# Kernel optimization log

Measured on AMD Instinct MI355X. Metric: run time of the kernel, lower is better.

The kernel has to match this reference:

```python
import jax, jax.numpy as jnp
import numpy as np

B, S, HID = 2, 2048, 2048
NH, NKV, HD = 8, 1, 256
G = NH // NKV  # key-value groups
ROPE_BASE = 10000.0


def _rope_tables(seq_len, dim, base=ROPE_BASE):
    inv_freq = 1.0 / (base ** (jnp.arange(0, dim, 2, dtype=jnp.float32) / dim))
    t = jnp.arange(seq_len, dtype=jnp.float32)
    freqs = jnp.outer(t, inv_freq)            # [S, dim/2]
    emb = jnp.concatenate([freqs, freqs], -1)  # [S, dim]
    return jnp.cos(emb), jnp.sin(emb)


def _rotate_half(x):
    x1, x2 = jnp.split(x, 2, axis=-1)
    return jnp.concatenate([-x2, x1], axis=-1)


def setup_inputs() -> dict:
    key = jax.random.key(0)
    ks = jax.random.split(key, 6)
    hidden_states = jax.random.normal(ks[0], (B, S, HID), dtype=jnp.float32)
    # additive causal mask (0 on/below diagonal, -1e9 above)
    causal = jnp.triu(jnp.full((S, S), -1e9, dtype=jnp.float32), k=1)
    attention_mask = jnp.broadcast_to(causal[None, None], (B, 1, S, S))
    sc = 0.02
    Wq = jax.random.normal(ks[1], (HID, NH * HD), dtype=jnp.float32) * sc
    Wk = jax.random.normal(ks[2], (HID, NKV * HD), dtype=jnp.float32) * sc
    Wv = jax.random.normal(ks[3], (HID, NKV * HD), dtype=jnp.float32) * sc
    Wo = jax.random.normal(ks[4], (NH * HD, HID), dtype=jnp.float32) * sc
    return {"hidden_states": hidden_states, "attention_mask": attention_mask,
            "Wq": Wq, "Wk": Wk, "Wv": Wv, "Wo": Wo}


def reference(hidden_states, attention_mask, Wq, Wk, Wv, Wo):
    b, s, _ = hidden_states.shape
    q = (hidden_states @ Wq).reshape(b, s, NH, HD).transpose(0, 2, 1, 3)    # [B,NH,S,D]
    k = (hidden_states @ Wk).reshape(b, s, NKV, HD).transpose(0, 2, 1, 3)   # [B,NKV,S,D]
    v = (hidden_states @ Wv).reshape(b, s, NKV, HD).transpose(0, 2, 1, 3)
    cos, sin = _rope_tables(s, HD)
    cos, sin = cos[None, None], sin[None, None]
    q = q * cos + _rotate_half(q) * sin
    k = k * cos + _rotate_half(k) * sin
    # GQA: broadcast KV over groups instead of repeat_interleave (same math)
    qg = q.reshape(b, NKV, G, s, HD)
    scores = jnp.einsum('bkgqd,bkld->bkgql', qg, k) / np.sqrt(HD)  # [B,NKV,G,S,S]
    scores = scores + attention_mask[:, :, None]                    # mask broadcast over kv/groups
    probs = jax.nn.softmax(scores, axis=-1)
    out = jnp.einsum('bkgql,bkld->bkgqd', probs, v)                 # [B,NKV,G,S,D]
    out = out.reshape(b, NH, s, HD).transpose(0, 2, 1, 3).reshape(b, s, NH * HD)
    return out @ Wo
```

## Files before the change

### kernel.cpp

```cpp
#include <hip/hip_runtime.h>
#include <hip/hip_bf16.h>
#include <cstdint>
#include <cstddef>

#define DEVI __device__ __forceinline__

typedef __attribute__((ext_vector_type(8))) short short8;
typedef __attribute__((ext_vector_type(4))) float f32x4;

constexpr int BB = 2, SS = 2048, HID = 2048, NH = 8, HD = 256;
constexpr int M_TOT = BB * SS;
constexpr int RTOT = BB * NH * SS;
constexpr float SM_SCALE_LOG2 = 0.09016844005556021f;

DEVI unsigned short f2bf(float f) {
  union { float f; unsigned int u; } v; v.f = f;
  unsigned int u = v.u;
  unsigned int r = (u + 0x7FFFu + ((u >> 16) & 1u)) >> 16;
  return (unsigned short)r;
}

DEVI float bf2f(unsigned short u) {
  union { unsigned int i; float f; } v; v.i = ((unsigned int)u) << 16;
  return v.f;
}

DEVI void gload_lds16(const void* g, void* l) {
  __builtin_amdgcn_global_load_lds(
      (const __attribute__((address_space(1))) unsigned int*)g,
      (__attribute__((address_space(3))) unsigned int*)l, 16, 0, 0);
}

__global__ void convert_f32_bf16(const float* __restrict__ in,
                                 unsigned short* __restrict__ out, int n8) {
  const int i = blockIdx.x * blockDim.x + threadIdx.x;
  if (i >= n8) return;
  const f32x4* p = (const f32x4*)in;
  f32x4 a = p[i * 2], b = p[i * 2 + 1];
  short8 o;
#pragma unroll
  for (int j = 0; j < 4; ++j) {
    o[j] = (short)f2bf(a[j]);
    o[j + 4] = (short)f2bf(b[j]);
  }
  ((short8*)out)[i] = o;
}

__global__ void transpose_w(const float* __restrict__ W,
                            unsigned short* __restrict__ Wt, int K, int N) {
  __shared__ float t[32][33];
  const int n0 = blockIdx.x * 32, k0 = blockIdx.y * 32;
  const int c = threadIdx.x & 31, r8 = threadIdx.x >> 5;
#pragma unroll
  for (int i = 0; i < 4; ++i) {
    const int r = r8 + i * 8;
    t[r][c] = W[(size_t)(k0 + r) * N + n0 + c];
  }
  __syncthreads();
#pragma unroll
  for (int i = 0; i < 4; ++i) {
    const int r = r8 + i * 8;
    Wt[(size_t)(n0 + r) * K + k0 + c] = f2bf(t[c][r]);
  }
}

__global__ void rope_table(float* __restrict__ ct, float* __restrict__ st) {
  const int i = blockIdx.x * blockDim.x + threadIdx.x;
  const int s = i >> 7, d = i & 127;
  const float inv = __expf(-(float)d * (9.210340371976184f / 128.0f));
  const float ang = (float)s * inv;
  float sn, cs;
  sincosf(ang, &sn, &cs);
  ct[i] = cs;
  st[i] = sn;
}

__global__ void rope_apply(unsigned short* __restrict__ X, const float* __restrict__ ct,
                           const float* __restrict__ st, int heads, int stride, int total) {
  const int i = blockIdx.x * blockDim.x + threadIdx.x;
  if (i >= total) return;
  const int d = i & 127;
  const int t = i >> 7;
  const int hh = t % heads;
  const int row = t / heads;
  const int s = row & (SS - 1);
  const size_t base = (size_t)row * stride + (size_t)hh * HD;
  const float q1 = bf2f(X[base + d]), q2 = bf2f(X[base + d + 128]);
  const float cs = ct[s * 128 + d], sn = st[s * 128 + d];
  X[base + d] = f2bf(q1 * cs - q2 * sn);
  X[base + d + 128] = f2bf(q2 * cs + q1 * sn);
}

template <int WMODE>
__global__ __launch_bounds__(256)
void gemm_bt(const unsigned short* __restrict__ A,
             const unsigned short* __restrict__ Bt,
             void* __restrict__ Cp, void* __restrict__ Cp2, void* __restrict__ Cp3,
             int N, int K) {
  __shared__ unsigned short As[128 * 64];
  __shared__ unsigned short Bs[128 * 64];
  const int tid = threadIdx.x;
  const int wid = tid >> 6, lane = tid & 63;
  const int wr = wid >> 1, wc = wid & 1;
  const int l15 = lane & 15, lg = lane >> 4;
  const int m0 = blockIdx.y * 128, n0 = blockIdx.x * 128;
  const int lrow = lane >> 3, lch = lane & 7;
  f32x4 acc[4][4];
#pragma unroll
  for (int i = 0; i < 4; ++i)
#pragma unroll
    for (int j = 0; j < 4; ++j) acc[i][j] = f32x4{0.f, 0.f, 0.f, 0.f};
  const unsigned short* Ab = A + (size_t)m0 * K;
  const unsigned short* Bb = Bt + (size_t)n0 * K;
  for (int k0 = 0; k0 < K; k0 += 64) {
    __syncthreads();
#pragma unroll
    for (int i = 0; i < 4; ++i) {
      const int r0 = wid * 32 + i * 8;
      const int r = r0 + lrow;
      gload_lds16(Ab + (size_t)r * K + k0 + ((lch ^ (r & 7)) * 8), &As[r0 * 64]);
      gload_lds16(Bb + (size_t)r * K + k0 + ((lch ^ (r & 7)) * 8), &Bs[r0 * 64]);
    }
    asm volatile("s_waitcnt vmcnt(0)" ::: "memory");
    __syncthreads();
#pragma unroll
    for (int kk = 0; kk < 2; ++kk) {
      short8 a[4], b[4];
#pragma unroll
      for (int m = 0; m < 4; ++m) {
        const int row = wr * 64 + m * 16 + l15;
        a[m] = *(const short8*)&As[row * 64 + (((kk * 4 + lg) ^ (row & 7)) * 8)];
      }
#pragma unroll
      for (int n = 0; n < 4; ++n) {
        const int row = wc * 64 + n * 16 + l15;
        b[n] = *(const short8*)&Bs[row * 64 + (((kk * 4 + lg) ^ (row & 7)) * 8)];
      }
#pragma unroll
      for (int m = 0; m < 4; ++m)
#pragma unroll
        for (int n = 0; n < 4; ++n)
          acc[m][n] = __builtin_amdgcn_mfma_f32_16x16x32_bf16(a[m], b[n], acc[m][n], 0, 0, 0);
    }
  }
  const int row0 = m0 + wr * 64 + lg * 4;
  const int col0 = n0 + wc * 64 + l15;
#pragma unroll
  for (int m = 0; m < 4; ++m)
#pragma unroll
    for (int n = 0; n < 4; ++n)
#pragma unroll
      for (int r = 0; r < 4; ++r) {
        const int row = row0 + m * 16 + r;
        const int col = col0 + n * 16;
        const float v = acc[m][n][r];
        if (WMODE == 1) {
          ((float*)Cp)[(size_t)row * N + col] = v;
        } else {
          if (col < 2048)
            ((unsigned short*)Cp)[(size_t)row * 2048 + col] = f2bf(v);
          else if (col < 2304)
            ((unsigned short*)Cp2)[(size_t)row * 256 + (col - 2048)] = f2bf(v);
          else
            ((unsigned short*)Cp3)[((size_t)((row >> 11) * HD + (col - 2304))) * SS + (row & (SS - 1))] = f2bf(v);
        }
      }
}

__global__ __launch_bounds__(512)
void attn_split(const unsigned short* __restrict__ Q,
                const unsigned short* __restrict__ Kc,
                const unsigned short* __restrict__ Vt,
                unsigned short* __restrict__ Opart, float* __restrict__ Ml) {
  __shared__ unsigned short Ks[2][64 * 256];
  __shared__ unsigned short Vs[2][256 * 64];
  __shared__ unsigned short Ps[8][1024];
  const int tid = threadIdx.x;
  const int wid = tid >> 6, lane = tid & 63;
  const int l15 = lane & 15, lg = lane >> 4;
  const int pi = (int)blockIdx.x >> 1, s = (int)blockIdx.x & 1;
  const int h = blockIdx.y, b = blockIdx.z;
  const int qtA = pi, qtB = 15 - pi;

  short8 qf[8];
  f32x4 acc[16];
  float mrow[4], lrow[4];

  auto load_q = [&](int qt) {
    const int qrow = qt * 128 + wid * 16 + l15;
    const size_t qbase = ((size_t)(b * SS + qrow)) * (NH * HD) + (size_t)h * HD;
#pragma unroll
    for (int c = 0; c < 8; ++c)
      qf[c] = *(const short8*)&Q[qbase + c * 32 + lg * 8];
#pragma unroll
    for (int n = 0; n < 16; ++n) acc[n] = f32x4{0.f, 0.f, 0.f, 0.f};
#pragma unroll
    for (int r = 0; r < 4; ++r) { mrow[r] = -3e38f; lrow[r] = 0.f; }
  };

  auto write_part = [&](int qt) {
    const size_t rbase = ((size_t)(b * NH + h)) * SS + qt * 128 + wid * 16 + lg * 4;
#pragma unroll
    for (int n = 0; n < 16; ++n)
#pragma unroll
      for (int r = 0; r < 4; ++r)
        Opart[((size_t)s * RTOT + rbase + r) * 256 + n * 16 + l15] = f2bf(acc[n][r]);
    if (l15 == 0) {
#pragma unroll
      for (int r = 0; r < 4; ++r)
        ((float2*)Ml)[(size_t)s * RTOT + rbase + r] = float2{mrow[r], lrow[r]};
    }
  };

  auto stage = [&](int buf, int kv0) {
    unsigned short* KsB = &Ks[buf][0];
    unsigned short* VsB = &Vs[buf][0];
#pragma unroll
    for (int j = 0; j < 4; ++j) {
      {
        const int r0 = wid * 8 + j * 2;
        const int r = r0 + (lane >> 5), c = lane & 31;
        gload_lds16(Kc + ((size_t)(b * SS + kv0 + r)) * HD + ((c ^ (r & 7)) * 8),
                    &KsB[r0 * 256]);
      }
      {
        const int r0 = (wid * 4 + j) * 8;
        const int r = r0 + (lane >> 3), c = lane & 7;
        gload_lds16(Vt + ((size_t)(b * HD + r)) * SS + kv0 + ((c ^ (r & 7)) * 8),
                    &VsB[r0 * 64]);
      }
    }
  };

  auto compute = [&](int buf, int qt, int kv0) {
    const int wmax = qt * 128 + wid * 16 + 15;
    if (kv0 > wmax) return;
    const unsigned short* KsB = &Ks[buf][0];
    const unsigned short* VsB = &Vs[buf][0];
    f32x4 sf[4];
    __builtin_amdgcn_s_setprio(1);
#pragma unroll
    for (int t = 0; t < 4; ++t) {
      f32x4 sv = {0.f, 0.f, 0.f, 0.f};
      const int kvr = t * 16 + l15;
      const char* krow = (const char*)KsB + kvr * 512;
      const int sw = (kvr & 7) << 4;
#pragma unroll
      for (int c = 0; c < 8; ++c) {
        short8 bf = *(const short8*)(krow + ((c * 64 + lg * 16) ^ sw));
        sv = __builtin_amdgcn_mfma_f32_16x16x32_bf16(qf[c], bf, sv, 0, 0, 0);
      }
      sf[t] = sv;
    }
    __builtin_amdgcn_s_setprio(0);

    float pm[4] = {-3e38f, -3e38f, -3e38f, -3e38f};
    const int qr0 = qt * 128 + wid * 16 + lg * 4;
#pragma unroll
    for (int t = 0; t < 4; ++t) {
      const int kvc = kv0 + t * 16 + l15;
#pragma unroll
      for (int r = 0; r < 4; ++r) {
        float v = sf[t][r] * SM_SCALE_LOG2;
        v = (kvc > qr0 + r) ? -3e38f : v;
        sf[t][r] = v;
        pm[r] = fmaxf(pm[r], v);
      }
    }
    float scale[4];
    float growth = -3e38f;
#pragma unroll
    for (int r = 0; r < 4; ++r) {
      float v = pm[r];
      v = fmaxf(v, __shfl_xor(v, 1));
      v = fmaxf(v, __shfl_xor(v, 2));
      v = fmaxf(v, __shfl_xor(v, 4));
      v = fmaxf(v, __shfl_xor(v, 8));
      pm[r] = v;
      growth = fmaxf(growth, v - mrow[r]);
    }
    const bool norescale = __all(growth <= 0.f);
#pragma unroll
    for (int r = 0; r < 4; ++r) {
      const float mn = norescale ? mrow[r] : fmaxf(mrow[r], pm[r]);
      scale[r] = norescale ? 1.f : exp2f(mrow[r] - mn);
      mrow[r] = mn;
      float sum = 0.f;
#pragma unroll
      for (int t = 0; t < 4; ++t) {
        const float p = exp2f(sf[t][r] - mn);
        sf[t][r] = p;
        sum += p;
      }
      sum += __shfl_xor(sum, 1);
      sum += __shfl_xor(sum, 2);
      sum += __shfl_xor(sum, 4);
      sum += __shfl_xor(sum, 8);
      lrow[r] = lrow[r] * scale[r] + sum;
    }
    if (!norescale) {
#pragma unroll
      for (int n = 0; n < 16; ++n)
#pragma unroll
        for (int r = 0; r < 4; ++r) acc[n][r] *= scale[r];
    }

    char* pw = (char*)&Ps[wid][0];
#pragma unroll
    for (int t = 0; t < 4; ++t)
#pragma unroll
      for (int r = 0; r < 4; ++r) {
        const int q = lg * 4 + r;
        *(unsigned short*)(pw + q * 128 + (((t * 16 + l15) * 2) ^ ((q & 7) << 4))) =
            f2bf(sf[t][r]);
      }
    asm volatile("s_waitcnt lgkmcnt(0)" ::: "memory");
    short8 pf[2];
    {
      const char* pr = pw + l15 * 128;
      const int sw = (l15 & 7) << 4;
      pf[0] = *(const short8*)(pr + ((lg * 16) ^ sw));
      pf[1] = *(const short8*)(pr + ((64 + lg * 16) ^ sw));
    }
    __builtin_amdgcn_s_setprio(1);
#pragma unroll
    for (int n = 0; n < 16; ++n) {
      const int dr = n * 16 + l15;
      const char* vrow = (const char*)VsB + dr * 128;
      const int sw = (dr & 7) << 4;
      short8 v0 = *(const short8*)(vrow + ((lg * 16) ^ sw));
      short8 v1 = *(const short8*)(vrow + ((64 + lg * 16) ^ sw));
      acc[n] = __builtin_amdgcn_mfma_f32_16x16x32_bf16(pf[0], v0, acc[n], 0, 0, 0);
      acc[n] = __builtin_amdgcn_mfma_f32_16x16x32_bf16(pf[1], v1, acc[n], 0, 0, 0);
    }
    __builtin_amdgcn_s_setprio(0);
  };

  auto kv_of = [&](int i) {
    const int j = (i <= qtA) ? i : (i - qtA - 1);
    return (s + 2 * j) * 64;
  };

  load_q(qtA);
  stage(0, kv_of(0));
  asm volatile("s_waitcnt vmcnt(0)" ::: "memory");
  __syncthreads();
  int buf = 0;
  for (int i = 0; i < 17; ++i) {
    if (i + 1 < 17) stage(buf ^ 1, kv_of(i + 1));
    if (i == qtA + 1) {
      write_part(qtA);
      load_q(qtB);
    }
    const int qt = (i <= qtA) ? qtA : qtB;
    compute(buf, qt, kv_of(i));
    asm volatile("s_waitcnt vmcnt(0)" ::: "memory");
    __syncthreads();
    buf ^= 1;
  }
  write_part(qtB);
}

__global__ void merge_splits(const unsigned short* __restrict__ Opart,
                             const float* __restrict__ Ml,
                             unsigned short* __restrict__ AO) {
  const int gid = blockIdx.x * 256 + threadIdx.x;
  const int ridx = gid >> 5;
  const int d0 = (gid & 31) * 8;
  const float2 ab0 = ((const float2*)Ml)[ridx];
  const float2 ab1 = ((const float2*)Ml)[RTOT + ridx];
  const float M = fmaxf(ab0.x, ab1.x);
  const float w0 = exp2f(ab0.x - M), w1 = exp2f(ab1.x - M);
  const float inv = 1.f / (w0 * ab0.y + w1 * ab1.y);
  const short8 p0 = *(const short8*)&Opart[(size_t)ridx * 256 + d0];
  const short8 p1 = *(const short8*)&Opart[((size_t)RTOT + ridx) * 256 + d0];
  const int b = ridx >> 14, rem = ridx & 16383;
  const int h = rem >> 11, srow = rem & 2047;
  short8 o;
#pragma unroll
  for (int j = 0; j < 8; ++j)
    o[j] = (short)f2bf((w0 * bf2f((unsigned short)p0[j]) +
                        w1 * bf2f((unsigned short)p1[j])) * inv);
  *(short8*)(AO + ((size_t)(b * SS + srow)) * (NH * HD) + (size_t)h * HD + d0) = o;
}

__global__ __launch_bounds__(256)
void attn_fb(const unsigned short* __restrict__ Q,
             const unsigned short* __restrict__ Kc,
             const unsigned short* __restrict__ Vt,
             unsigned short* __restrict__ AO) {
  __shared__ unsigned short Ks[2][64 * 256];
  __shared__ unsigned short Vs[2][256 * 64];
  __shared__ unsigned short Ps[4][1024];
  const int tid = threadIdx.x;
  const int wid = tid >> 6, lane = tid & 63;
  const int l15 = lane & 15, lg = lane >> 4;
  const int qtA = (int)blockIdx.x;
  const int qtB = 31 - qtA;
  const int h = blockIdx.y, b = blockIdx.z;

  short8 qf[8];
  f32x4 acc[16];
  float mrow[4], lrow[4];

  auto load_q = [&](int qt) {
    const int qrow = qt * 64 + wid * 16 + l15;
    const size_t qbase = ((size_t)(b * SS + qrow)) * (NH * HD) + (size_t)h * HD;
#pragma unroll
    for (int c = 0; c < 8; ++c)
      qf[c] = *(const short8*)&Q[qbase + c * 32 + lg * 8];
#pragma unroll
    for (int n = 0; n < 16; ++n) acc[n] = f32x4{0.f, 0.f, 0.f, 0.f};
#pragma unroll
    for (int r = 0; r < 4; ++r) { mrow[r] = -3e38f; lrow[r] = 0.f; }
  };

  auto write_o = [&](int qt) {
    float invl[4];
#pragma unroll
    for (int r = 0; r < 4; ++r) invl[r] = 1.f / lrow[r];
    const int orow0 = b * SS + qt * 64 + wid * 16 + lg * 4;
#pragma unroll
    for (int n = 0; n < 16; ++n)
#pragma unroll
      for (int r = 0; r < 4; ++r)
        AO[(size_t)(orow0 + r) * (NH * HD) + (size_t)h * HD + n * 16 + l15] =
            f2bf(acc[n][r] * invl[r]);
  };

  auto stage = [&](int buf, int kv0) {
    unsigned short* KsB = &Ks[buf][0];
    unsigned short* VsB = &Vs[buf][0];
#pragma unroll
    for (int j = 0; j < 8; ++j) {
      {
        const int r0 = wid * 16 + j * 2;
        const int r = r0 + (lane >> 5), c = lane & 31;
        gload_lds16(Kc + ((size_t)(b * SS + kv0 + r)) * HD + ((c ^ (r & 7)) * 8),
                    &KsB[r0 * 256]);
      }
      {
        const int r0 = (wid * 8 + j) * 8;
        const int r = r0 + (lane >> 3), c = lane & 7;
        gload_lds16(Vt + ((size_t)(b * HD + r)) * SS + kv0 + ((c ^ (r & 7)) * 8),
                    &VsB[r0 * 64]);
      }
    }
  };

  auto compute = [&](int buf, int qt, int kv0) {
    const int wmax = qt * 64 + wid * 16 + 15;
    if (kv0 > wmax) return;
    const unsigned short* KsB = &Ks[buf][0];
    const unsigned short* VsB = &Vs[buf][0];
    f32x4 sf[4];
#pragma unroll
    for (int t = 0; t < 4; ++t) {
      f32x4 sv = {0.f, 0.f, 0.f, 0.f};
      const int kvr = t * 16 + l15;
      const char* krow = (const char*)KsB + kvr * 512;
      const int sw = (kvr & 7) << 4;
#pragma unroll
      for (int c = 0; c < 8; ++c) {
        short8 bf = *(const short8*)(krow + ((c * 64 + lg * 16) ^ sw));
        sv = __builtin_amdgcn_mfma_f32_16x16x32_bf16(qf[c], bf, sv, 0, 0, 0);
      }
      sf[t] = sv;
    }
    float pm[4] = {-3e38f, -3e38f, -3e38f, -3e38f};
    const int qr0 = qt * 64 + wid * 16 + lg * 4;
#pragma unroll
    for (int t = 0; t < 4; ++t) {
      const int kvc = kv0 + t * 16 + l15;
#pragma unroll
      for (int r = 0; r < 4; ++r) {
        float v = sf[t][r] * 0.0625f;
        v = (kvc > qr0 + r) ? -3e38f : v;
        sf[t][r] = v;
        pm[r] = fmaxf(pm[r], v);
      }
    }
    float scale[4];
    float growth = -3e38f;
#pragma unroll
    for (int r = 0; r < 4; ++r) {
      float v = pm[r];
      v = fmaxf(v, __shfl_xor(v, 1));
      v = fmaxf(v, __shfl_xor(v, 2));
      v = fmaxf(v, __shfl_xor(v, 4));
      v = fmaxf(v, __shfl_xor(v, 8));
      pm[r] = v;
      growth = fmaxf(growth, v - mrow[r]);
    }
    const bool norescale = __all(growth <= 0.f);
#pragma unroll
    for (int r = 0; r < 4; ++r) {
      const float mn = norescale ? mrow[r] : fmaxf(mrow[r], pm[r]);
      scale[r] = norescale ? 1.f : __expf(mrow[r] - mn);
      mrow[r] = mn;
      float sum = 0.f;
#pragma unroll
      for (int t = 0; t < 4; ++t) {
        const float p = __expf(sf[t][r] - mn);
        sf[t][r] = p;
        sum += p;
      }
      sum += __shfl_xor(sum, 1);
      sum += __shfl_xor(sum, 2);
      sum += __shfl_xor(sum, 4);
      sum += __shfl_xor(sum, 8);
      lrow[r] = lrow[r] * scale[r] + sum;
    }
    if (!norescale) {
#pragma unroll
      for (int n = 0; n < 16; ++n)
#pragma unroll
        for (int r = 0; r < 4; ++r) acc[n][r] *= scale[r];
    }
    char* pw = (char*)&Ps[wid][0];
#pragma unroll
    for (int t = 0; t < 4; ++t)
#pragma unroll
      for (int r = 0; r < 4; ++r) {
        const int q = lg * 4 + r;
        *(unsigned short*)(pw + q * 128 + (((t * 16 + l15) * 2) ^ ((q & 7) << 4))) =
            f2bf(sf[t][r]);
      }
    asm volatile("s_waitcnt lgkmcnt(0)" ::: "memory");
    short8 pf[2];
    {
      const char* pr = pw + l15 * 128;
      const int sw = (l15 & 7) << 4;
      pf[0] = *(const short8*)(pr + ((lg * 16) ^ sw));
      pf[1] = *(const short8*)(pr + ((64 + lg * 16) ^ sw));
    }
#pragma unroll
    for (int n = 0; n < 16; ++n) {
      const int dr = n * 16 + l15;
      const char* vrow = (const char*)VsB + dr * 128;
      const int sw = (dr & 7) << 4;
      short8 v0 = *(const short8*)(vrow + ((lg * 16) ^ sw));
      short8 v1 = *(const short8*)(vrow + ((64 + lg * 16) ^ sw));
      acc[n] = __builtin_amdgcn_mfma_f32_16x16x32_bf16(pf[0], v0, acc[n], 0, 0, 0);
      acc[n] = __builtin_amdgcn_mfma_f32_16x16x32_bf16(pf[1], v1, acc[n], 0, 0, 0);
    }
  };

  const int nA = qtA + 1;
  load_q(qtA);
  int curq = qtA;
  stage(0, 0);
  asm volatile("s_waitcnt vmcnt(0)" ::: "memory");
  __syncthreads();
  int buf = 0;
  for (int i = 0; i < 33; ++i) {
    const int t0 = (i >= nA) ? (i - nA) : i;
    if (i + 1 < 33) {
      const int t0n = (i + 1 >= nA) ? (i + 1 - nA) : (i + 1);
      stage(buf ^ 1, t0n * 64);
    }
    if (i >= nA && curq == qtA) {
      write_o(qtA);
      load_q(qtB);
      curq = qtB;
    }
    compute(buf, curq, t0 * 64);
    asm volatile("s_waitcnt vmcnt(0)" ::: "memory");
    __syncthreads();
    buf ^= 1;
  }
  write_o(qtB);
}

extern "C" void kernel_launch(void* const* d_in, const int* in_sizes, int n_in,
                              void* d_out, int out_size, void* d_ws, size_t ws_size,
                              hipStream_t stream) {
  (void)in_sizes; (void)n_in; (void)out_size;
  const float* hs = (const float*)d_in[0];
  const float* Wq = (const float*)d_in[2];
  const float* Wk = (const float*)d_in[3];
  const float* Wv = (const float*)d_in[4];
  const float* Wo = (const float*)d_in[5];

  char* ws = (char*)d_ws;
  size_t off = 0;
  auto alloc = [&](size_t bytes) -> void* {
    void* p = ws + off;
    off += (bytes + 255) & ~(size_t)255;
    return p;
  };
  unsigned short* Xb  = (unsigned short*)alloc((size_t)M_TOT * HID * 2);
  unsigned short* WqT = (unsigned short*)alloc((size_t)2048 * 2048 * 2);
  unsigned short* WkT = (unsigned short*)alloc((size_t)256 * 2048 * 2);
  unsigned short* WvT = (unsigned short*)alloc((size_t)256 * 2048 * 2);
  unsigned short* WoT = (unsigned short*)alloc((size_t)2048 * 2048 * 2);
  unsigned short* Qb  = (unsigned short*)alloc((size_t)M_TOT * 2048 * 2);
  unsigned short* Kb  = (unsigned short*)alloc((size_t)M_TOT * 256 * 2);
  unsigned short* Vtw = (unsigned short*)alloc((size_t)M_TOT * 256 * 2);
  float* ct = (float*)alloc((size_t)SS * 128 * 4);
  float* st = (float*)alloc((size_t)SS * 128 * 4);
  unsigned short* Opart = (unsigned short*)alloc((size_t)2 * RTOT * 256 * 2);
  float* Mlb = (float*)alloc((size_t)2 * RTOT * 2 * 4);
  const bool use_split = ws_size >= off;
  unsigned short* AO = Xb;

  convert_f32_bf16<<<M_TOT * HID / 8 / 256, 256, 0, stream>>>(hs, Xb, M_TOT * HID / 8);
  transpose_w<<<dim3(2048 / 32, 2048 / 32), 256, 0, stream>>>(Wq, WqT, 2048, 2048);
  transpose_w<<<dim3(256 / 32, 2048 / 32), 256, 0, stream>>>(Wk, WkT, 2048, 256);
  transpose_w<<<dim3(256 / 32, 2048 / 32), 256, 0, stream>>>(Wv, WvT, 2048, 256);
  transpose_w<<<dim3(2048 / 32, 2048 / 32), 256, 0, stream>>>(Wo, WoT, 2048, 2048);
  rope_table<<<SS * 128 / 256, 256, 0, stream>>>(ct, st);

  gemm_bt<4><<<dim3(2560 / 128, M_TOT / 128), 256, 0, stream>>>(Xb, WqT, Qb, Kb, Vtw, 2560, 2048);

  rope_apply<<<(M_TOT * NH * 128) / 256, 256, 0, stream>>>(Qb, ct, st, NH, 2048, M_TOT * NH * 128);
  rope_apply<<<(M_TOT * 128) / 256, 256, 0, stream>>>(Kb, ct, st, 1, 256, M_TOT * 128);

  if (use_split) {
    attn_split<<<dim3(16, NH, BB), 512, 0, stream>>>(Qb, Kb, Vtw, Opart, Mlb);
    merge_splits<<<RTOT * 32 / 256, 256, 0, stream>>>(Opart, Mlb, AO);
  } else {
    attn_fb<<<dim3(16, NH, BB), 256, 0, stream>>>(Qb, Kb, Vtw, AO);
  }

  gemm_bt<1><<<dim3(2048 / 128, M_TOT / 128), 256, 0, stream>>>(AO, WoT, d_out, nullptr, nullptr, 2048, 2048);
}
```

Baseline: 237.1 us.

## Vectorize RoPE apply, swizzle GEMM block order, drop attention setprio

The RoPE kernel now processes 8 bf16 elements per thread, using 16-byte loads and stores for the activations and float4 loads for the cos/sin tables. This cuts instruction count and memory transactions. The GEMM remaps linear block IDs so that consecutive blocks are spread across eight groups (likely targeting the XCDs) to improve L2 locality. The attention kernel drops its s_setprio raises around the MFMA sections, which changes wave scheduling priority and could help or hurt.

```diff
diff --git a/kernel.cpp b/kernel.cpp
--- a/kernel.cpp
+++ b/kernel.cpp
@@ -75,20 +75,34 @@
   st[i] = sn;
 }
 
-__global__ void rope_apply(unsigned short* __restrict__ X, const float* __restrict__ ct,
-                           const float* __restrict__ st, int heads, int stride, int total) {
+__global__ void rope_apply8(unsigned short* __restrict__ X, const float* __restrict__ ct,
+                            const float* __restrict__ st, int heads, int stride, int total16) {
   const int i = blockIdx.x * blockDim.x + threadIdx.x;
-  if (i >= total) return;
-  const int d = i & 127;
-  const int t = i >> 7;
+  if (i >= total16) return;
+  const int d0 = (i & 15) * 8;
+  const int t = i >> 4;
   const int hh = t % heads;
   const int row = t / heads;
   const int s = row & (SS - 1);
-  const size_t base = (size_t)row * stride + (size_t)hh * HD;
-  const float q1 = bf2f(X[base + d]), q2 = bf2f(X[base + d + 128]);
-  const float cs = ct[s * 128 + d], sn = st[s * 128 + d];
-  X[base + d] = f2bf(q1 * cs - q2 * sn);
-  X[base + d + 128] = f2bf(q2 * cs + q1 * sn);
+  const size_t base = (size_t)row * stride + (size_t)hh * HD + d0;
+  short8 q1 = *(const short8*)&X[base];
+  short8 q2 = *(const short8*)&X[base + 128];
+  const float* ctr = ct + s * 128 + d0;
+  const float* str = st + s * 128 + d0;
+  f32x4 c0 = *(const f32x4*)ctr, c1 = *(const f32x4*)(ctr + 4);
+  f32x4 s0 = *(const f32x4*)str, s1 = *(const f32x4*)(str + 4);
+  short8 o1, o2;
+#pragma unroll
+  for (int j = 0; j < 8; ++j) {
+    const float a = bf2f((unsigned short)q1[j]);
+    const float b = bf2f((unsigned short)q2[j]);
+    const float cs = (j < 4) ? c0[j] : c1[j - 4];
+    const float sn = (j < 4) ? s0[j] : s1[j - 4];
+    o1[j] = (short)f2bf(a * cs - b * sn);
+    o2[j] = (short)f2bf(b * cs + a * sn);
+  }
+  *(short8*)&X[base] = o1;
+  *(short8*)&X[base + 128] = o2;
 }
 
 template <int WMODE>
@@ -103,7 +117,10 @@
   const int wid = tid >> 6, lane = tid & 63;
   const int wr = wid >> 1, wc = wid & 1;
   const int l15 = lane & 15, lg = lane >> 4;
-  const int m0 = blockIdx.y * 128, n0 = blockIdx.x * 128;
+  const unsigned lid = blockIdx.y * gridDim.x + blockIdx.x;
+  const unsigned cpx = (gridDim.x * gridDim.y) >> 3;
+  const unsigned swz = (lid & 7) * cpx + (lid >> 3);
+  const int m0 = (int)(swz / gridDim.x) * 128, n0 = (int)(swz % gridDim.x) * 128;
   const int lrow = lane >> 3, lch = lane & 7;
   f32x4 acc[4][4];
 #pragma unroll
@@ -238,7 +255,6 @@
     const unsigned short* KsB = &Ks[buf][0];
     const unsigned short* VsB = &Vs[buf][0];
     f32x4 sf[4];
-    __builtin_amdgcn_s_setprio(1);
 #pragma unroll
     for (int t = 0; t < 4; ++t) {
       f32x4 sv = {0.f, 0.f, 0.f, 0.f};
@@ -252,7 +268,6 @@
       }
       sf[t] = sv;
     }
-    __builtin_amdgcn_s_setprio(0);
 
     float pm[4] = {-3e38f, -3e38f, -3e38f, -3e38f};
     const int qr0 = qt * 128 + wid * 16 + lg * 4;
@@ -322,7 +337,6 @@
       pf[0] = *(const short8*)(pr + ((lg * 16) ^ sw));
       pf[1] = *(const short8*)(pr + ((64 + lg * 16) ^ sw));
     }
-    __builtin_amdgcn_s_setprio(1);
 #pragma unroll
     for (int n = 0; n < 16; ++n) {
       const int dr = n * 16 + l15;
@@ -333,7 +347,6 @@
       acc[n] = __builtin_amdgcn_mfma_f32_16x16x32_bf16(pf[0], v0, acc[n], 0, 0, 0);
       acc[n] = __builtin_amdgcn_mfma_f32_16x16x32_bf16(pf[1], v1, acc[n], 0, 0, 0);
     }
-    __builtin_amdgcn_s_setprio(0);
   };
 
   auto kv_of = [&](int i) {
@@ -613,8 +626,8 @@
 
   gemm_bt<4><<<dim3(2560 / 128, M_TOT / 128), 256, 0, stream>>>(Xb, WqT, Qb, Kb, Vtw, 2560, 2048);
 
-  rope_apply<<<(M_TOT * NH * 128) / 256, 256, 0, stream>>>(Qb, ct, st, NH, 2048, M_TOT * NH * 128);
-  rope_apply<<<(M_TOT * 128) / 256, 256, 0, stream>>>(Kb, ct, st, 1, 256, M_TOT * 128);
+  rope_apply8<<<(M_TOT * NH * 16) / 256, 256, 0, stream>>>(Qb, ct, st, NH, 2048, M_TOT * NH * 16);
+  rope_apply8<<<(M_TOT * 16) / 256, 256, 0, stream>>>(Kb, ct, st, 1, 256, M_TOT * 16);
 
   if (use_split) {
     attn_split<<<dim3(16, NH, BB), 512, 0, stream>>>(Qb, Kb, Vtw, Opart, Mlb);
```

New measurement: 234.5 us. Within noise of the previous version (-1.1%).
